# Performance work log

Measured on AMD Instinct MI355X. Metric: run time of the kernel, lower is better.

Reference implementation:

```python
import jax, jax.numpy as jnp
import numpy as np

N_NODES = 100000
N_EDGES = 1000000
D_IN, D_HID, D_OUT = 64, 64, 64


def _glorot(key, shape):
    fan_in, fan_out = shape[1], shape[0]
    lim = (6.0 / (fan_in + fan_out)) ** 0.5
    return jax.random.uniform(key, shape, jnp.float32, -lim, lim)


def setup_inputs() -> dict:
    key = jax.random.key(0)
    ks = jax.random.split(key, 8)
    x = jax.random.normal(ks[0], (N_NODES, D_IN), dtype=jnp.float32)
    edge_index = jax.random.randint(ks[1], (2, N_EDGES), 0, N_NODES, dtype=jnp.int64)
    # SAGEConv params: lin_l (applied to aggregated neighbors, has bias), lin_r (root, no bias)
    W1l = _glorot(ks[2], (D_HID, D_IN)); b1l = jnp.zeros((D_HID,), jnp.float32)
    W1r = _glorot(ks[3], (D_HID, D_IN))
    W2l = _glorot(ks[4], (D_OUT, D_HID)); b2l = jnp.zeros((D_OUT,), jnp.float32)
    W2r = _glorot(ks[5], (D_OUT, D_HID))
    return {"x": x, "edge_index": edge_index,
            "W1l": W1l, "b1l": b1l, "W1r": W1r,
            "W2l": W2l, "b2l": b2l, "W2r": W2r}


def _sage_conv(x, src, dst, Wl, bl, Wr, num_nodes):
    # gather source features, scatter-mean onto destinations
    msg = x[src]                                        # [E, d]
    agg = jax.ops.segment_sum(msg, dst, num_segments=num_nodes)   # [N, d]
    cnt = jax.ops.segment_sum(jnp.ones((src.shape[0],), x.dtype), dst,
                              num_segments=num_nodes)   # [N]
    mean = agg / jnp.maximum(cnt, 1.0)[:, None]
    # out = lin_l(mean_neighbors) + lin_r(x)
    return mean @ Wl.T + bl + x @ Wr.T


def reference(x, edge_index, W1l, b1l, W1r, W2l, b2l, W2r):
    src, dst = edge_index[0], edge_index[1]
    n = x.shape[0]
    h = jax.nn.relu(_sage_conv(x, src, dst, W1l, b1l, W1r, n))
    out = _sage_conv(h, src, dst, W2l, b2l, W2r, n)
    return out
```

## Files before the change

### kernel.cpp

```cpp
#include <hip/hip_runtime.h>

#define N_NODES 100000
#define N_EDGES 1000000
#define D 64
#define NB 196
#define SUBCAP 1024
#define BSTAGE 6144
#define CHUNK 4096
#define ABLOCKS ((N_EDGES + CHUNK - 1) / CHUNK)
#define NTILES (N_NODES / 16)
#define LING 768

typedef __attribute__((ext_vector_type(8))) __bf16 bf16x8;
typedef __attribute__((ext_vector_type(4))) float f32x4;

__device__ __forceinline__ unsigned short f2b(float f) {
    unsigned u = __float_as_uint(f);
    unsigned r = u + 0x7FFFu + ((u >> 16) & 1u);
    return (unsigned short)(r >> 16);
}
__device__ __forceinline__ float blo(unsigned u) {
    return __uint_as_float(u << 16);
}
__device__ __forceinline__ float bhi(unsigned u) {
    return __uint_as_float(u & 0xFFFF0000u);
}
__device__ __forceinline__ unsigned pack2(float a, float b) {
    return (unsigned)f2b(a) | ((unsigned)f2b(b) << 16);
}

__device__ __forceinline__ void split8(float4 p, float4 q, uint4& hv, uint4& lv) {
    float e[8] = {p.x, p.y, p.z, p.w, q.x, q.y, q.z, q.w};
    unsigned hb[8], lb[8];
#pragma unroll
    for (int i = 0; i < 8; i++) {
        unsigned u = __float_as_uint(e[i]);
        unsigned hf = u & 0xFFFF0000u;
        hb[i] = u >> 16;
        lb[i] = f2b(e[i] - __uint_as_float(hf));
    }
    hv.x = hb[0] | (hb[1] << 16); hv.y = hb[2] | (hb[3] << 16);
    hv.z = hb[4] | (hb[5] << 16); hv.w = hb[6] | (hb[7] << 16);
    lv.x = lb[0] | (lb[1] << 16); lv.y = lb[2] | (lb[3] << 16);
    lv.z = lb[4] | (lb[5] << 16); lv.w = lb[6] | (lb[7] << 16);
}

__global__ void __launch_bounds__(256)
k_bucketA(const int* __restrict__ ei, int* __restrict__ subcur,
          int* __restrict__ pairs) {
    __shared__ int hist[256];
    __shared__ int sc[256];
    __shared__ int lpos[NB];
    __shared__ int lcur[NB];
    __shared__ int gbase[NB];
    __shared__ int stage[CHUNK];
    __shared__ int astage[CHUNK];
    int t = threadIdx.x, blk = blockIdx.x;
    int sub = blk & 7;
    int e0 = blk * CHUNK;
    int e1 = min(e0 + CHUNK, N_EDGES);
    int cnt = e1 - e0;

    hist[t] = 0;
    __syncthreads();
    for (int i = t; i < cnt; i += 256) {
        int d = ei[N_EDGES + e0 + i];
        atomicAdd(&hist[d >> 9], 1);
    }
    __syncthreads();
    int h = hist[t];
    sc[t] = h;
    __syncthreads();
    for (int off = 1; off < 256; off <<= 1) {
        int v = (t >= off) ? sc[t - off] : 0;
        __syncthreads();
        sc[t] += v;
        __syncthreads();
    }
    if (t < NB) {
        int excl = sc[t] - h;
        lpos[t] = excl;
        lcur[t] = excl;
        gbase[t] = (h > 0) ? atomicAdd(&subcur[(t << 3) | sub], h) : 0;
    }
    __syncthreads();
    for (int i = t; i < cnt; i += 256) {
        int s = ei[e0 + i];
        int d = ei[N_EDGES + e0 + i];
        int b = d >> 9;
        int p = atomicAdd(&lcur[b], 1);
        int o = gbase[b] + (p - lpos[b]);
        stage[p] = (s << 9) | (d & 511);
        astage[p] = (o < SUBCAP) ? (((b << 3) | sub) * SUBCAP + o) : -1;
    }
    __syncthreads();
    for (int i = t; i < cnt; i += 256) {
        int a = astage[i];
        if (a >= 0) pairs[a] = stage[i];
    }
}

__global__ void k_bscan(const int* __restrict__ subcur, int* __restrict__ bucket_base) {
    __shared__ int tot[256];
    int t = threadIdx.x;
    int sum = 0;
    if (t < NB) {
        for (int s = 0; s < 8; s++) sum += min(subcur[t * 8 + s], SUBCAP);
    }
    tot[t] = sum;
    __syncthreads();
    for (int off = 1; off < 256; off <<= 1) {
        int v = (t >= off) ? tot[t - off] : 0;
        __syncthreads();
        tot[t] += v;
        __syncthreads();
    }
    if (t < NB) bucket_base[t] = (t == 0) ? 0 : tot[t - 1];
    if (t == NB - 1) bucket_base[NB] = tot[t];
}

__global__ void __launch_bounds__(256)
k_bucketB(const int* __restrict__ subcur, const int* __restrict__ pairs,
          const int* __restrict__ bucket_base, int* __restrict__ col,
          int* __restrict__ row_start, float* __restrict__ invc) {
    __shared__ int ldeg[512];
    __shared__ int lpos[512];
    __shared__ int lcur[512];
    __shared__ int sc[256];
    __shared__ int cnt[8];
    __shared__ int stage[BSTAGE];
    int b = blockIdx.x, t = threadIdx.x;
    if (t < 8) cnt[t] = min(subcur[b * 8 + t], SUBCAP);
    for (int i = t; i < 512; i += 256) ldeg[i] = 0;
    __syncthreads();
    for (int s = 0; s < 8; s++) {
        int c = cnt[s];
        const int* base = pairs + (size_t)(b * 8 + s) * SUBCAP;
        for (int i = t; i < c; i += 256) atomicAdd(&ldeg[base[i] & 511], 1);
    }
    __syncthreads();
    int a0 = ldeg[2 * t], a1 = ldeg[2 * t + 1];
    sc[t] = a0 + a1;
    __syncthreads();
    for (int off = 1; off < 256; off <<= 1) {
        int v = (t >= off) ? sc[t - off] : 0;
        __syncthreads();
        sc[t] += v;
        __syncthreads();
    }
    int excl = (t == 0) ? 0 : sc[t - 1];
    lpos[2 * t] = excl;
    lpos[2 * t + 1] = excl + a0;
    lcur[2 * t] = excl;
    lcur[2 * t + 1] = excl + a0;
    __syncthreads();
    int bbase = bucket_base[b];
    int total = bucket_base[b + 1] - bbase;
    if (total > BSTAGE) total = BSTAGE;
    int n0 = b * 512;
    for (int i = t; i < 512; i += 256) {
        int n = n0 + i;
        if (n < N_NODES) {
            row_start[n] = bbase + lpos[i];
            int dg = ldeg[i];
            invc[n] = 1.0f / (float)(dg > 0 ? dg : 1);
        }
    }
    if (b == 0 && t == 0) row_start[N_NODES] = bucket_base[NB];
    for (int s = 0; s < 8; s++) {
        int c = cnt[s];
        const int* base = pairs + (size_t)(b * 8 + s) * SUBCAP;
        for (int i = t; i < c; i += 256) {
            int v = base[i];
            int p = atomicAdd(&lcur[v & 511], 1);
            if (p < BSTAGE) stage[p] = v >> 9;
        }
    }
    __syncthreads();
    for (int i = t; i < total; i += 256) col[bbase + i] = stage[i];
}

__global__ void __launch_bounds__(256)
k_cast(const float4* __restrict__ X4, uint4* __restrict__ Xb) {
    int i = blockIdx.x * 256 + threadIdx.x;
    if (i >= N_NODES * D / 8) return;
    float4 a = X4[2 * i];
    float4 b = X4[2 * i + 1];
    uint4 o;
    o.x = pack2(a.x, a.y);
    o.y = pack2(a.z, a.w);
    o.z = pack2(b.x, b.y);
    o.w = pack2(b.z, b.w);
    Xb[i] = o;
}

__global__ void __launch_bounds__(256)
k_agg_b(const uint4* __restrict__ Xb, const int* __restrict__ row_start,
        const int* __restrict__ col, const float* __restrict__ inv_cnt,
        float4* __restrict__ M4) {
    int t = blockIdx.x * 256 + threadIdx.x;
    int sub = t & 7;
    int n = t >> 3;
    if (n >= N_NODES) return;
    int s = row_start[n];
    int e = row_start[n + 1];
    float a[8];
#pragma unroll
    for (int i = 0; i < 8; i++) a[i] = 0.f;
    int j = s;
    for (; j + 4 <= e; j += 4) {
        int c0 = col[j + 0];
        int c1 = col[j + 1];
        int c2 = col[j + 2];
        int c3 = col[j + 3];
        uint4 q0 = Xb[(size_t)c0 * 8 + sub];
        uint4 q1 = Xb[(size_t)c1 * 8 + sub];
        uint4 q2 = Xb[(size_t)c2 * 8 + sub];
        uint4 q3 = Xb[(size_t)c3 * 8 + sub];
        const unsigned* u0 = (const unsigned*)&q0;
        const unsigned* u1 = (const unsigned*)&q1;
        const unsigned* u2 = (const unsigned*)&q2;
        const unsigned* u3 = (const unsigned*)&q3;
#pragma unroll
        for (int w = 0; w < 4; w++) {
            a[2 * w + 0] += (blo(u0[w]) + blo(u1[w])) + (blo(u2[w]) + blo(u3[w]));
            a[2 * w + 1] += (bhi(u0[w]) + bhi(u1[w])) + (bhi(u2[w]) + bhi(u3[w]));
        }
    }
    for (; j < e; j++) {
        uint4 q = Xb[(size_t)col[j] * 8 + sub];
        const unsigned* u = (const unsigned*)&q;
#pragma unroll
        for (int w = 0; w < 4; w++) {
            a[2 * w + 0] += blo(u[w]);
            a[2 * w + 1] += bhi(u[w]);
        }
    }
    float ic = inv_cnt[n];
    M4[(size_t)n * 16 + sub * 2 + 0] = make_float4(a[0] * ic, a[1] * ic,
                                                   a[2] * ic, a[3] * ic);
    M4[(size_t)n * 16 + sub * 2 + 1] = make_float4(a[4] * ic, a[5] * ic,
                                                   a[6] * ic, a[7] * ic);
}

__global__ void __launch_bounds__(256, 3)
k_linear_mfma(const float* __restrict__ Ma, const float* __restrict__ Xa,
              const float* __restrict__ Wl, const float* __restrict__ Wr,
              const float* __restrict__ bias, float* __restrict__ out,
              int do_relu, uint2* __restrict__ xb_out) {
    __shared__ uint4 wH[4][4][64];
    __shared__ uint4 wL[4][4][64];
    int t = threadIdx.x;

    for (int idx = t; idx < 1024; idx += 256) {
        int lane = idx & 63;
        int ot = (idx >> 6) & 3;
        int kb = idx >> 8;
        int oc = ot * 16 + (lane & 15);
        int kk = kb * 32 + (lane >> 4) * 8;
        const float* src = (kk < 64) ? (Wl + oc * 64 + kk)
                                     : (Wr + oc * 64 + (kk - 64));
        float4 p = *(const float4*)src;
        float4 q = *(const float4*)(src + 4);
        uint4 hv, lv;
        split8(p, q, hv, lv);
        wH[kb][ot][lane] = hv;
        wL[kb][ot][lane] = lv;
    }
    __syncthreads();

    int lane = t & 63;
    int wv = t >> 6;
    int nin = lane & 15;
    int kg = lane >> 4;

    float4 bq[4];
#pragma unroll
    for (int ot = 0; ot < 4; ot++)
        bq[ot] = *(const float4*)(bias + ot * 16 + kg * 4);

    for (int tile = blockIdx.x * 4 + wv; tile < NTILES; tile += (int)gridDim.x * 4) {
        size_t n = (size_t)tile * 16 + nin;
        const float4* mp = (const float4*)Ma + n * 16 + kg * 2;
        const float4* xp = (const float4*)Xa + n * 16 + kg * 2;
        float4 r0 = mp[0], r1 = mp[1], r2 = mp[8], r3 = mp[9];
        float4 r4 = xp[0], r5 = xp[1], r6 = xp[8], r7 = xp[9];

        f32x4 acc[4];
#pragma unroll
        for (int ot = 0; ot < 4; ot++) {
            f32x4 a;
            a[0] = bq[ot].x; a[1] = bq[ot].y; a[2] = bq[ot].z; a[3] = bq[ot].w;
            acc[ot] = a;
        }

        uint4 ahv[4], alv[4];
        split8(r0, r1, ahv[0], alv[0]);
        split8(r2, r3, ahv[1], alv[1]);
        split8(r4, r5, ahv[2], alv[2]);
        split8(r6, r7, ahv[3], alv[3]);

#pragma unroll
        for (int kb = 0; kb < 4; kb++) {
            bf16x8 ah = __builtin_bit_cast(bf16x8, ahv[kb]);
            bf16x8 al = __builtin_bit_cast(bf16x8, alv[kb]);
#pragma unroll
            for (int ot = 0; ot < 4; ot++) {
                bf16x8 wh = __builtin_bit_cast(bf16x8, wH[kb][ot][lane]);
                bf16x8 wl = __builtin_bit_cast(bf16x8, wL[kb][ot][lane]);
                acc[ot] = __builtin_amdgcn_mfma_f32_16x16x32_bf16(wh, ah, acc[ot], 0, 0, 0);
                acc[ot] = __builtin_amdgcn_mfma_f32_16x16x32_bf16(wh, al, acc[ot], 0, 0, 0);
                acc[ot] = __builtin_amdgcn_mfma_f32_16x16x32_bf16(wl, ah, acc[ot], 0, 0, 0);
            }
        }

#pragma unroll
        for (int ot = 0; ot < 4; ot++) {
            float v0 = acc[ot][0], v1 = acc[ot][1], v2 = acc[ot][2], v3 = acc[ot][3];
            if (do_relu) {
                v0 = fmaxf(v0, 0.f); v1 = fmaxf(v1, 0.f);
                v2 = fmaxf(v2, 0.f); v3 = fmaxf(v3, 0.f);
            }
            *(float4*)(out + n * 64 + ot * 16 + kg * 4) = make_float4(v0, v1, v2, v3);
            if (xb_out) {
                *(uint2*)((unsigned*)xb_out + n * 32 + ot * 8 + kg * 2) =
                    make_uint2(pack2(v0, v1), pack2(v2, v3));
            }
        }
    }
}

extern "C" void kernel_launch(void* const* d_in, const int* in_sizes, int n_in,
                              void* d_out, int out_size, void* d_ws, size_t ws_size,
                              hipStream_t stream) {
    const float* x   = (const float*)d_in[0];
    const int*   ei  = (const int*)d_in[1];
    const float* W1l = (const float*)d_in[2];
    const float* b1  = (const float*)d_in[3];
    const float* W1r = (const float*)d_in[4];
    const float* W2l = (const float*)d_in[5];
    const float* b2  = (const float*)d_in[6];
    const float* W2r = (const float*)d_in[7];
    float* out = (float*)d_out;

    char* ws = (char*)d_ws;
    size_t off = 0;
    auto alloc = [&](size_t bytes) -> char* {
        char* p = ws + off;
        off = (off + bytes + 255) & ~(size_t)255;
        return p;
    };
    int*   row_start   = (int*)alloc((size_t)(N_NODES + 1) * 4);
    int*   col         = (int*)alloc((size_t)N_EDGES * 4);
    float* invc        = (float*)alloc((size_t)N_NODES * 4);
    int*   subcur      = (int*)alloc((size_t)NB * 8 * 4);
    int*   bucket_base = (int*)alloc((size_t)(NB + 1) * 4);
    char*  region      = alloc((size_t)N_NODES * D * 2);
    float* mbuf        = (float*)alloc((size_t)N_NODES * D * 4);
    float* hbuf        = (float*)alloc((size_t)N_NODES * D * 4);
    int*   pairs = (int*)region;
    uint4* xb    = (uint4*)region;

    hipMemsetAsync(subcur, 0, (size_t)NB * 8 * 4, stream);
    k_bucketA<<<ABLOCKS, 256, 0, stream>>>(ei, subcur, pairs);
    k_bscan<<<1, 256, 0, stream>>>(subcur, bucket_base);
    k_bucketB<<<NB, 256, 0, stream>>>(subcur, pairs, bucket_base, col, row_start, invc);

    const int cast_blocks = (N_NODES * D / 8 + 255) / 256;
    const int agg_blocks  = (N_NODES * 8 + 255) / 256;

    k_cast<<<cast_blocks, 256, 0, stream>>>((const float4*)x, xb);
    k_agg_b<<<agg_blocks, 256, 0, stream>>>(xb, row_start, col, invc, (float4*)mbuf);
    k_linear_mfma<<<LING, 256, 0, stream>>>(mbuf, x, W1l, W1r, b1, hbuf, 1, (uint2*)xb);
    k_agg_b<<<agg_blocks, 256, 0, stream>>>(xb, row_start, col, invc, (float4*)mbuf);
    k_linear_mfma<<<LING, 256, 0, stream>>>(mbuf, hbuf, W2l, W2r, b2, out, 0, nullptr);
}
```

Before: 237.4 us.

## Fuse neighbor aggregation into MFMA linear kernel via per-wave LDS staging

Merges the gather/mean aggregation kernel with the MFMA linear kernel. Each wave aggregates a 16-node tile (4 lanes per node, 16 features each), stages the mean rows in LDS, then runs the split-bf16 MFMA on them. This removes the fp32 mean buffer round trip through global memory and two launches. Layer 1 now writes its bf16 copy to a separate buffer, so it no longer overwrites the input the other waves are still gathering from. The trade-off is lower gather parallelism per wave (fewer lanes per node, a persistent grid with a strided tile start) and extra LDS use, which may hurt latency hiding for the irregular gathers.

```diff
diff --git a/kernel.cpp b/kernel.cpp
--- a/kernel.cpp
+++ b/kernel.cpp
@@ -9,7 +9,8 @@
 #define CHUNK 4096
 #define ABLOCKS ((N_EDGES + CHUNK - 1) / CHUNK)
 #define NTILES (N_NODES / 16)
-#define LING 768
+#define FB 768
+#define FW (FB * 4)
 
 typedef __attribute__((ext_vector_type(8))) __bf16 bf16x8;
 typedef __attribute__((ext_vector_type(4))) float f32x4;
@@ -194,62 +195,57 @@
     Xb[i] = o;
 }
 
-__global__ void __launch_bounds__(256)
-k_agg_b(const uint4* __restrict__ Xb, const int* __restrict__ row_start,
-        const int* __restrict__ col, const float* __restrict__ inv_cnt,
-        float4* __restrict__ M4) {
-    int t = blockIdx.x * 256 + threadIdx.x;
-    int sub = t & 7;
-    int n = t >> 3;
-    if (n >= N_NODES) return;
-    int s = row_start[n];
-    int e = row_start[n + 1];
-    float a[8];
-#pragma unroll
-    for (int i = 0; i < 8; i++) a[i] = 0.f;
-    int j = s;
-    for (; j + 4 <= e; j += 4) {
-        int c0 = col[j + 0];
-        int c1 = col[j + 1];
-        int c2 = col[j + 2];
-        int c3 = col[j + 3];
-        uint4 q0 = Xb[(size_t)c0 * 8 + sub];
-        uint4 q1 = Xb[(size_t)c1 * 8 + sub];
-        uint4 q2 = Xb[(size_t)c2 * 8 + sub];
-        uint4 q3 = Xb[(size_t)c3 * 8 + sub];
-        const unsigned* u0 = (const unsigned*)&q0;
-        const unsigned* u1 = (const unsigned*)&q1;
-        const unsigned* u2 = (const unsigned*)&q2;
-        const unsigned* u3 = (const unsigned*)&q3;
-#pragma unroll
-        for (int w = 0; w < 4; w++) {
-            a[2 * w + 0] += (blo(u0[w]) + blo(u1[w])) + (blo(u2[w]) + blo(u3[w]));
-            a[2 * w + 1] += (bhi(u0[w]) + bhi(u1[w])) + (bhi(u2[w]) + bhi(u3[w]));
-        }
-    }
-    for (; j < e; j++) {
-        uint4 q = Xb[(size_t)col[j] * 8 + sub];
-        const unsigned* u = (const unsigned*)&q;
-#pragma unroll
-        for (int w = 0; w < 4; w++) {
-            a[2 * w + 0] += blo(u[w]);
-            a[2 * w + 1] += bhi(u[w]);
-        }
-    }
-    float ic = inv_cnt[n];
-    M4[(size_t)n * 16 + sub * 2 + 0] = make_float4(a[0] * ic, a[1] * ic,
-                                                   a[2] * ic, a[3] * ic);
-    M4[(size_t)n * 16 + sub * 2 + 1] = make_float4(a[4] * ic, a[5] * ic,
-                                                   a[6] * ic, a[7] * ic);
+__device__ __forceinline__ void lin_tile(
+    const uint4 ahv[4], const uint4 alv[4],
+    const uint4 (*wHp)[4][64], const uint4 (*wLp)[4][64],
+    const float4 bq[4], int lane, int kg, size_t n,
+    float* __restrict__ out, unsigned* __restrict__ xb_out, int do_relu)
+{
+    f32x4 acc[4];
+#pragma unroll
+    for (int ot = 0; ot < 4; ot++) {
+        f32x4 a;
+        a[0] = bq[ot].x; a[1] = bq[ot].y; a[2] = bq[ot].z; a[3] = bq[ot].w;
+        acc[ot] = a;
+    }
+#pragma unroll
+    for (int kb = 0; kb < 4; kb++) {
+        bf16x8 ah = __builtin_bit_cast(bf16x8, ahv[kb]);
+        bf16x8 al = __builtin_bit_cast(bf16x8, alv[kb]);
+#pragma unroll
+        for (int ot = 0; ot < 4; ot++) {
+            bf16x8 wh = __builtin_bit_cast(bf16x8, wHp[kb][ot][lane]);
+            bf16x8 wl = __builtin_bit_cast(bf16x8, wLp[kb][ot][lane]);
+            acc[ot] = __builtin_amdgcn_mfma_f32_16x16x32_bf16(wh, ah, acc[ot], 0, 0, 0);
+            acc[ot] = __builtin_amdgcn_mfma_f32_16x16x32_bf16(wh, al, acc[ot], 0, 0, 0);
+            acc[ot] = __builtin_amdgcn_mfma_f32_16x16x32_bf16(wl, ah, acc[ot], 0, 0, 0);
+        }
+    }
+#pragma unroll
+    for (int ot = 0; ot < 4; ot++) {
+        float v0 = acc[ot][0], v1 = acc[ot][1], v2 = acc[ot][2], v3 = acc[ot][3];
+        if (do_relu) {
+            v0 = fmaxf(v0, 0.f); v1 = fmaxf(v1, 0.f);
+            v2 = fmaxf(v2, 0.f); v3 = fmaxf(v3, 0.f);
+        }
+        *(float4*)(out + n * 64 + ot * 16 + kg * 4) = make_float4(v0, v1, v2, v3);
+        if (xb_out) {
+            *(uint2*)(xb_out + n * 32 + ot * 8 + kg * 2) =
+                make_uint2(pack2(v0, v1), pack2(v2, v3));
+        }
+    }
 }
 
 __global__ void __launch_bounds__(256, 3)
-k_linear_mfma(const float* __restrict__ Ma, const float* __restrict__ Xa,
-              const float* __restrict__ Wl, const float* __restrict__ Wr,
-              const float* __restrict__ bias, float* __restrict__ out,
-              int do_relu, uint2* __restrict__ xb_out) {
+k_agg_lin(const uint4* __restrict__ Xb, const float* __restrict__ Xa,
+          const int* __restrict__ row_start, const int* __restrict__ col,
+          const float* __restrict__ invc,
+          const float* __restrict__ Wl, const float* __restrict__ Wr,
+          const float* __restrict__ bias, float* __restrict__ out,
+          int do_relu, unsigned* __restrict__ xb_out) {
     __shared__ uint4 wH[4][4][64];
     __shared__ uint4 wL[4][4][64];
+    __shared__ float mrow[4][16 * 68];
     int t = threadIdx.x;
 
     for (int idx = t; idx < 1024; idx += 256) {
@@ -273,60 +269,91 @@
     int wv = t >> 6;
     int nin = lane & 15;
     int kg = lane >> 4;
+    int na = lane >> 2;
+    int sub4 = lane & 3;
+    float* ms = mrow[wv];
 
     float4 bq[4];
 #pragma unroll
     for (int ot = 0; ot < 4; ot++)
         bq[ot] = *(const float4*)(bias + ot * 16 + kg * 4);
 
-    for (int tile = blockIdx.x * 4 + wv; tile < NTILES; tile += (int)gridDim.x * 4) {
-        size_t n = (size_t)tile * 16 + nin;
-        const float4* mp = (const float4*)Ma + n * 16 + kg * 2;
-        const float4* xp = (const float4*)Xa + n * 16 + kg * 2;
-        float4 r0 = mp[0], r1 = mp[1], r2 = mp[8], r3 = mp[9];
-        float4 r4 = xp[0], r5 = xp[1], r6 = xp[8], r7 = xp[9];
-
-        f32x4 acc[4];
-#pragma unroll
-        for (int ot = 0; ot < 4; ot++) {
-            f32x4 a;
-            a[0] = bq[ot].x; a[1] = bq[ot].y; a[2] = bq[ot].z; a[3] = bq[ot].w;
-            acc[ot] = a;
-        }
+    int w = blockIdx.x * 4 + wv;
+    int t0 = (w * 7) % FW;
+    for (int tile = t0; tile < NTILES; tile += FW) {
+        int nagg = tile * 16 + na;
+        int s = row_start[nagg];
+        int e = row_start[nagg + 1];
+        float ic = invc[nagg];
+        size_t nlin = (size_t)tile * 16 + nin;
+
+        const float4* xp = (const float4*)Xa + nlin * 16 + kg * 2;
+        float4 x0 = xp[0], x1 = xp[1], x2 = xp[8], x3 = xp[9];
+
+        float a[16];
+#pragma unroll
+        for (int i = 0; i < 16; i++) a[i] = 0.f;
+        int cb = 2 * sub4;
+        int j = s;
+        for (; j + 4 <= e; j += 4) {
+            int c0 = col[j + 0], c1 = col[j + 1], c2 = col[j + 2], c3 = col[j + 3];
+            uint4 q0a = Xb[(size_t)c0 * 8 + cb], q0b = Xb[(size_t)c0 * 8 + cb + 1];
+            uint4 q1a = Xb[(size_t)c1 * 8 + cb], q1b = Xb[(size_t)c1 * 8 + cb + 1];
+            uint4 q2a = Xb[(size_t)c2 * 8 + cb], q2b = Xb[(size_t)c2 * 8 + cb + 1];
+            uint4 q3a = Xb[(size_t)c3 * 8 + cb], q3b = Xb[(size_t)c3 * 8 + cb + 1];
+            const unsigned* u0a = (const unsigned*)&q0a;
+            const unsigned* u1a = (const unsigned*)&q1a;
+            const unsigned* u2a = (const unsigned*)&q2a;
+            const unsigned* u3a = (const unsigned*)&q3a;
+            const unsigned* u0b = (const unsigned*)&q0b;
+            const unsigned* u1b = (const unsigned*)&q1b;
+            const unsigned* u2b = (const unsigned*)&q2b;
+            const unsigned* u3b = (const unsigned*)&q3b;
+#pragma unroll
+            for (int wd = 0; wd < 4; wd++) {
+                a[2 * wd + 0] += (blo(u0a[wd]) + blo(u1a[wd])) + (blo(u2a[wd]) + blo(u3a[wd]));
+                a[2 * wd + 1] += (bhi(u0a[wd]) + bhi(u1a[wd])) + (bhi(u2a[wd]) + bhi(u3a[wd]));
+                a[8 + 2 * wd + 0] += (blo(u0b[wd]) + blo(u1b[wd])) + (blo(u2b[wd]) + blo(u3b[wd]));
+                a[8 + 2 * wd + 1] += (bhi(u0b[wd]) + bhi(u1b[wd])) + (bhi(u2b[wd]) + bhi(u3b[wd]));
+            }
+        }
+        for (; j < e; j++) {
+            int c = col[j];
+            uint4 qa = Xb[(size_t)c * 8 + cb], qb = Xb[(size_t)c * 8 + cb + 1];
+            const unsigned* ua = (const unsigned*)&qa;
+            const unsigned* ub = (const unsigned*)&qb;
+#pragma unroll
+            for (int wd = 0; wd < 4; wd++) {
+                a[2 * wd + 0] += blo(ua[wd]);
+                a[2 * wd + 1] += bhi(ua[wd]);
+                a[8 + 2 * wd + 0] += blo(ub[wd]);
+                a[8 + 2 * wd + 1] += bhi(ub[wd]);
+            }
+        }
+
+        int wb = na * 68 + sub4 * 16;
+#pragma unroll
+        for (int i4 = 0; i4 < 4; i4++) {
+            *(float4*)&ms[wb + i4 * 4] = make_float4(a[i4 * 4 + 0] * ic, a[i4 * 4 + 1] * ic,
+                                                     a[i4 * 4 + 2] * ic, a[i4 * 4 + 3] * ic);
+        }
+        asm volatile("s_waitcnt lgkmcnt(0)" ::: "memory");
+        __builtin_amdgcn_sched_barrier(0);
 
         uint4 ahv[4], alv[4];
-        split8(r0, r1, ahv[0], alv[0]);
-        split8(r2, r3, ahv[1], alv[1]);
-        split8(r4, r5, ahv[2], alv[2]);
-        split8(r6, r7, ahv[3], alv[3]);
-
-#pragma unroll
-        for (int kb = 0; kb < 4; kb++) {
-            bf16x8 ah = __builtin_bit_cast(bf16x8, ahv[kb]);
-            bf16x8 al = __builtin_bit_cast(bf16x8, alv[kb]);
-#pragma unroll
-            for (int ot = 0; ot < 4; ot++) {
-                bf16x8 wh = __builtin_bit_cast(bf16x8, wH[kb][ot][lane]);
-                bf16x8 wl = __builtin_bit_cast(bf16x8, wL[kb][ot][lane]);
-                acc[ot] = __builtin_amdgcn_mfma_f32_16x16x32_bf16(wh, ah, acc[ot], 0, 0, 0);
-                acc[ot] = __builtin_amdgcn_mfma_f32_16x16x32_bf16(wh, al, acc[ot], 0, 0, 0);
-                acc[ot] = __builtin_amdgcn_mfma_f32_16x16x32_bf16(wl, ah, acc[ot], 0, 0, 0);
-            }
-        }
-
-#pragma unroll
-        for (int ot = 0; ot < 4; ot++) {
-            float v0 = acc[ot][0], v1 = acc[ot][1], v2 = acc[ot][2], v3 = acc[ot][3];
-            if (do_relu) {
-                v0 = fmaxf(v0, 0.f); v1 = fmaxf(v1, 0.f);
-                v2 = fmaxf(v2, 0.f); v3 = fmaxf(v3, 0.f);
-            }
-            *(float4*)(out + n * 64 + ot * 16 + kg * 4) = make_float4(v0, v1, v2, v3);
-            if (xb_out) {
-                *(uint2*)((unsigned*)xb_out + n * 32 + ot * 8 + kg * 2) =
-                    make_uint2(pack2(v0, v1), pack2(v2, v3));
-            }
-        }
+        {
+            int rb = nin * 68 + kg * 8;
+            float4 m0 = *(const float4*)&ms[rb + 0];
+            float4 m1 = *(const float4*)&ms[rb + 4];
+            float4 m2 = *(const float4*)&ms[rb + 32];
+            float4 m3 = *(const float4*)&ms[rb + 36];
+            split8(m0, m1, ahv[0], alv[0]);
+            split8(m2, m3, ahv[1], alv[1]);
+        }
+        split8(x0, x1, ahv[2], alv[2]);
+        split8(x2, x3, ahv[3], alv[3]);
+
+        lin_tile(ahv, alv, wH, wL, bq, lane, kg, nlin, out, xb_out, do_relu);
     }
 }
 
@@ -356,10 +383,11 @@
     int*   subcur      = (int*)alloc((size_t)NB * 8 * 4);
     int*   bucket_base = (int*)alloc((size_t)(NB + 1) * 4);
     char*  region      = alloc((size_t)N_NODES * D * 2);
-    float* mbuf        = (float*)alloc((size_t)N_NODES * D * 4);
+    char*  xb2region   = alloc((size_t)N_NODES * D * 2);
     float* hbuf        = (float*)alloc((size_t)N_NODES * D * 4);
     int*   pairs = (int*)region;
     uint4* xb    = (uint4*)region;
+    uint4* xb2   = (uint4*)xb2region;
 
     hipMemsetAsync(subcur, 0, (size_t)NB * 8 * 4, stream);
     k_bucketA<<<ABLOCKS, 256, 0, stream>>>(ei, subcur, pairs);
@@ -367,11 +395,10 @@
     k_bucketB<<<NB, 256, 0, stream>>>(subcur, pairs, bucket_base, col, row_start, invc);
 
     const int cast_blocks = (N_NODES * D / 8 + 255) / 256;
-    const int agg_blocks  = (N_NODES * 8 + 255) / 256;
 
     k_cast<<<cast_blocks, 256, 0, stream>>>((const float4*)x, xb);
-    k_agg_b<<<agg_blocks, 256, 0, stream>>>(xb, row_start, col, invc, (float4*)mbuf);
-    k_linear_mfma<<<LING, 256, 0, stream>>>(mbuf, x, W1l, W1r, b1, hbuf, 1, (uint2*)xb);
-    k_agg_b<<<agg_blocks, 256, 0, stream>>>(xb, row_start, col, invc, (float4*)mbuf);
-    k_linear_mfma<<<LING, 256, 0, stream>>>(mbuf, hbuf, W2l, W2r, b2, out, 0, nullptr);
-}
+    k_agg_lin<<<FB, 256, 0, stream>>>(xb, x, row_start, col, invc,
+                                      W1l, W1r, b1, hbuf, 1, (unsigned*)xb2);
+    k_agg_lin<<<FB, 256, 0, stream>>>(xb2, hbuf, row_start, col, invc,
+                                      W2l, W2r, b2, out, 0, nullptr);
+}
```

Measured after the change: 204.9 us. 1.16x faster.
